# Kernel tuning notes

Hardware: AMD Instinct MI355X
Metric: run time of the kernel (lower is better)

## Reference

```python
import jax, jax.numpy as jnp
import numpy as np

D_MODEL = 1024
NUM_HEADS = 16
DEPTH = D_MODEL // NUM_HEADS
USE_MASKING = True


def setup_inputs() -> dict:
    key = jax.random.key(0)
    k1, k2, k3, k4 = jax.random.split(key, 4)
    B, S = 2, 2048
    x = jax.random.normal(k1, (B, S, D_MODEL), dtype=jnp.float32)
    # qkv_proj: Linear(d_model, 3*d_model, bias=False); torch stores W as [out, in]
    W_qkv = jax.random.normal(k2, (3 * D_MODEL, D_MODEL), dtype=jnp.float32) * (1.0 / np.sqrt(D_MODEL))
    W_out = jax.random.normal(k3, (D_MODEL, D_MODEL), dtype=jnp.float32) * (1.0 / np.sqrt(D_MODEL))
    b_out = jax.random.normal(k4, (D_MODEL,), dtype=jnp.float32) * 0.01
    return {"x": x, "W_qkv": W_qkv, "W_out": W_out, "b_out": b_out}


def reference(x, W_qkv, W_out, b_out):
    B, S, _ = x.shape
    qkv = jnp.einsum('bsd,ed->bse', x, W_qkv)  # [B,S,3*d_model]
    q, k, v = jnp.split(qkv, 3, axis=-1)
    # [B,S,H,depth] -> [B,H,S,depth]
    def heads(t):
        return t.reshape(B, S, NUM_HEADS, DEPTH).transpose(0, 2, 1, 3)
    q, k, v = heads(q), heads(k), heads(v)
    scores = jnp.einsum('bhqd,bhkd->bhqk', q, k) / np.sqrt(DEPTH).astype(np.float32)
    if USE_MASKING:
        mask = jnp.triu(jnp.ones((S, S), dtype=bool), k=1)
        scores = jnp.where(mask, -jnp.inf, scores)
    attn = jax.nn.softmax(scores, axis=-1)
    out = jnp.einsum('bhqk,bhkd->bhqd', attn, v)
    out = out.transpose(0, 2, 1, 3).reshape(B, S, D_MODEL)
    return jnp.einsum('bsd,ed->bse', out, W_out) + b_out
```

## Files before the change

kernel.cpp:

```cpp
#include <hip/hip_runtime.h>
#include <stdint.h>

typedef __attribute__((ext_vector_type(8))) short bf16x8;
typedef __attribute__((ext_vector_type(4))) float f32x4;
typedef __attribute__((ext_vector_type(4))) unsigned short u16x4;

#define AS1 __attribute__((address_space(1)))
#define AS3 __attribute__((address_space(3)))

#define BATCH 2
#define SEQ   2048
#define DMODEL 1024
#define NHEAD 16
#define DHEAD 64
#define QKVLD 3072
#define MROWS (BATCH*SEQ)

__device__ short g_xb   [MROWS * DMODEL];
__device__ short g_wqkv [3*DMODEL * DMODEL];
__device__ short g_wout [DMODEL * DMODEL];
__device__ short g_qkv  [(size_t)MROWS * QKVLD];
__device__ short g_attno[MROWS * DMODEL];

__device__ __forceinline__ unsigned short f2bf(float f) {
  union { float f; unsigned u; } v; v.f = f;
  unsigned r = v.u + 0x7FFFu + ((v.u >> 16) & 1u);
  return (unsigned short)(r >> 16);
}
__device__ __forceinline__ float bf2f(short s) {
  union { unsigned u; float f; } v; v.u = ((unsigned)(unsigned short)s) << 16;
  return v.f;
}
__device__ __forceinline__ void gload_lds16(const void* g, void* l) {
  __builtin_amdgcn_global_load_lds((const AS1 void*)(uintptr_t)g,
                                   (AS3 void*)(uint32_t)(uintptr_t)l, 16, 0, 0);
}

__global__ void cvt3(const float* __restrict__ x, const float* __restrict__ wq,
                     const float* __restrict__ wo) {
  const int N0 = MROWS * DMODEL;
  const int N1 = 3 * DMODEL * DMODEL;
  const int N2 = DMODEL * DMODEL;
  const int total = N0 + N1 + N2;
  int i = (blockIdx.x * blockDim.x + threadIdx.x) * 4;
  const int stride = gridDim.x * blockDim.x * 4;
  for (; i < total; i += stride) {
    const float* src; short* dst; int off;
    if (i < N0)           { src = x;  dst = g_xb;   off = i; }
    else if (i < N0 + N1) { src = wq; dst = g_wqkv; off = i - N0; }
    else                  { src = wo; dst = g_wout; off = i - N0 - N1; }
    float4 v = *reinterpret_cast<const float4*>(src + off);
    u16x4 o = { f2bf(v.x), f2bf(v.y), f2bf(v.z), f2bf(v.w) };
    *reinterpret_cast<u16x4*>(dst + off) = o;
  }
}

__device__ __forceinline__ void gemm_body(const short* __restrict__ A,
                                          const short* __restrict__ B,
                                          short* __restrict__ Cb,
                                          float* __restrict__ Cf,
                                          const float* __restrict__ bias,
                                          int N, int K, int bx, int by) {
  __shared__ short As[128 * 32];
  __shared__ short Bs[128 * 32];
  const int tid  = threadIdx.x;
  const int lane = tid & 63;
  const int wid  = tid >> 6;
  const int wr = wid >> 1, wc = wid & 1;
  const int g = lane >> 4, c = lane & 15;
  const long row0 = (long)by * 128;
  const long col0 = (long)bx * 128;

  const short* gA = A + (row0 + wid * 32 + (lane >> 2)) * (long)K + (lane & 3) * 8;
  const short* gB = B + (col0 + wid * 32 + (lane >> 2)) * (long)K + (lane & 3) * 8;
  short* lA = As + wid * 1024;
  short* lB = Bs + wid * 1024;

  f32x4 acc[4][4];
  const f32x4 z = {0.f, 0.f, 0.f, 0.f};
#pragma unroll
  for (int i = 0; i < 4; i++)
#pragma unroll
    for (int j = 0; j < 4; j++) acc[i][j] = z;

  for (int kt = 0; kt < K; kt += 32) {
    __syncthreads();
    gload_lds16(gA + kt,                lA);
    gload_lds16(gA + kt + 16 * (long)K, lA + 512);
    gload_lds16(gB + kt,                lB);
    gload_lds16(gB + kt + 16 * (long)K, lB + 512);
    __syncthreads();

    bf16x8 af[4], bfr[4];
#pragma unroll
    for (int mf = 0; mf < 4; mf++)
      af[mf] = *reinterpret_cast<const bf16x8*>(As + (wr * 64 + mf * 16 + c) * 32 + g * 8);
#pragma unroll
    for (int nf = 0; nf < 4; nf++)
      bfr[nf] = *reinterpret_cast<const bf16x8*>(Bs + (wc * 64 + nf * 16 + c) * 32 + g * 8);
#pragma unroll
    for (int mf = 0; mf < 4; mf++)
#pragma unroll
      for (int nf = 0; nf < 4; nf++)
        acc[mf][nf] = __builtin_amdgcn_mfma_f32_16x16x32_bf16(af[mf], bfr[nf], acc[mf][nf], 0, 0, 0);
  }

#pragma unroll
  for (int mf = 0; mf < 4; mf++)
#pragma unroll
    for (int nf = 0; nf < 4; nf++)
#pragma unroll
      for (int r = 0; r < 4; r++) {
        const long m = row0 + wr * 64 + mf * 16 + g * 4 + r;
        const long n = col0 + wc * 64 + nf * 16 + c;
        if (Cb) Cb[m * N + n] = (short)f2bf(acc[mf][nf][r]);
        else    Cf[m * N + n] = acc[mf][nf][r] + bias[n];
      }
}

__global__ __launch_bounds__(256) void gemm_qkv_k() {
  const int id = blockIdx.x;
  const int j = id >> 3;
  const int bx = j >> 2;
  const int by = ((id & 7) << 2) | (j & 3);
  gemm_body(g_xb, g_wqkv, g_qkv, nullptr, nullptr, 3 * DMODEL, DMODEL, bx, by);
}
__global__ __launch_bounds__(256) void gemm_out_k(float* __restrict__ out,
                                                  const float* __restrict__ bias) {
  const int id = blockIdx.x;
  const int j = id >> 3;
  const int bx = j >> 2;
  const int by = ((id & 7) << 2) | (j & 3);
  gemm_body(g_attno, g_wout, nullptr, out, bias, DMODEL, DMODEL, bx, by);
}

__global__ __launch_bounds__(256, 2) void flash_attn() {
  __shared__ short Kl[3][64 * 64];
  __shared__ short Vt[3][64 * 64];
  __shared__ short Pl[4][32 * 64];
  const int tid = threadIdx.x;
  const int lane = tid & 63, wid = tid >> 6;
  const int g = (lane >> 4) & 3, c = lane & 15;
  const int id = blockIdx.x;
  const int bh = id & 31;
  const int b = bh >> 4, h = bh & 15;
  const int qb = (id < 256) ? (15 - (id >> 5)) : ((id - 256) >> 5);
  const short* base = g_qkv + (size_t)b * SEQ * QKVLD + h * DHEAD;
  const int qw = qb * 128 + wid * 32;
  const int nt = 2 * qb + 2;

  const float QS = 0.18033688011112042f;
  bf16x8 qf[2][2];
#pragma unroll
  for (int n = 0; n < 2; n++)
#pragma unroll
    for (int kc = 0; kc < 2; kc++) {
      bf16x8 raw = *reinterpret_cast<const bf16x8*>(
          base + (size_t)(qw + n * 16 + c) * QKVLD + kc * 32 + g * 8);
#pragma unroll
      for (int j = 0; j < 8; j++) raw[j] = (short)f2bf(bf2f(raw[j]) * QS);
      qf[n][kc] = raw;
    }

  f32x4 oacc[2][4];
  const f32x4 z = {0.f, 0.f, 0.f, 0.f};
#pragma unroll
  for (int mq = 0; mq < 2; mq++)
#pragma unroll
    for (int nd = 0; nd < 4; nd++) oacc[mq][nd] = z;
  float mrow[2] = {-__builtin_inff(), -__builtin_inff()};
  float lrow[2] = {0.f, 0.f};

  const int srow = lane >> 3;
  const int scol = (lane & 7) ^ srow;
  const short* kgsrc = base + 1024 + (size_t)(wid * 16 + srow) * QKVLD + scol * 8;
  const short* vgsrc = base + 2048 + (size_t)lane * QKVLD + wid * 16;

  {
    bf16x8 a0 = *reinterpret_cast<const bf16x8*>(vgsrc);
    bf16x8 a1 = *reinterpret_cast<const bf16x8*>(vgsrc + 8);
    gload_lds16(kgsrc,                     &Kl[0][wid * 1024]);
    gload_lds16(kgsrc + (size_t)8 * QKVLD, &Kl[0][wid * 1024 + 512]);
    const size_t r1 = (size_t)64 * QKVLD;
    bf16x8 b0 = *reinterpret_cast<const bf16x8*>(vgsrc + r1);
    bf16x8 b1 = *reinterpret_cast<const bf16x8*>(vgsrc + r1 + 8);
    gload_lds16(kgsrc + r1,                     &Kl[1][wid * 1024]);
    gload_lds16(kgsrc + r1 + (size_t)8 * QKVLD, &Kl[1][wid * 1024 + 512]);
#pragma unroll
    for (int j = 0; j < 8; j++) {
      Vt[0][(wid * 16 + j) * 64 + (lane ^ (j << 3))] = a0[j];
      Vt[0][(wid * 16 + 8 + j) * 64 + (lane ^ (j << 3))] = a1[j];
    }
#pragma unroll
    for (int j = 0; j < 8; j++) {
      Vt[1][(wid * 16 + j) * 64 + (lane ^ (j << 3))] = b0[j];
      Vt[1][(wid * 16 + 8 + j) * 64 + (lane ^ (j << 3))] = b1[j];
    }
    asm volatile("s_waitcnt lgkmcnt(0)" ::: "memory");
    __builtin_amdgcn_sched_barrier(0);
    __builtin_amdgcn_s_barrier();
    asm volatile("" ::: "memory");
  }

  int cur = 0;
  for (int t = 0; t < nt; t++) {
    const int sidx = (cur + 2 >= 3) ? cur - 1 : cur + 2;
    const bool sl = (t + 2 < nt);
    bf16x8 vr0, vr1;
    if (sl) {
      const size_t roff = (size_t)(t + 2) * 64 * QKVLD;
      vr0 = *reinterpret_cast<const bf16x8*>(vgsrc + roff);
      vr1 = *reinterpret_cast<const bf16x8*>(vgsrc + roff + 8);
      gload_lds16(kgsrc + roff,                     &Kl[sidx][wid * 1024]);
      gload_lds16(kgsrc + roff + (size_t)8 * QKVLD, &Kl[sidx][wid * 1024 + 512]);
    }
    const int k0 = t * 64;
    if (k0 <= qw + 31) {
      f32x4 sc[4][2];
      __builtin_amdgcn_s_setprio(1);
#pragma unroll
      for (int m = 0; m < 4; m++) {
        const short* kr = &Kl[cur][(m * 16 + c) * 64];
        bf16x8 ka0 = *reinterpret_cast<const bf16x8*>(kr + ((g ^ (c & 7)) << 3));
        bf16x8 ka1 = *reinterpret_cast<const bf16x8*>(kr + (((4 + g) ^ (c & 7)) << 3));
#pragma unroll
        for (int n = 0; n < 2; n++) {
          f32x4 s = __builtin_amdgcn_mfma_f32_16x16x32_bf16(ka0, qf[n][0], z, 0, 0, 0);
          s = __builtin_amdgcn_mfma_f32_16x16x32_bf16(ka1, qf[n][1], s, 0, 0, 0);
          sc[m][n] = s;
        }
      }
      __builtin_amdgcn_s_setprio(0);
      if (k0 + 63 > qw) {
#pragma unroll
        for (int m = 0; m < 4; m++)
#pragma unroll
          for (int n = 0; n < 2; n++)
#pragma unroll
            for (int r = 0; r < 4; r++)
              if (k0 + m * 16 + g * 4 + r > qw + n * 16 + c)
                sc[m][n][r] = -__builtin_inff();
      }
      float tm[2];
#pragma unroll
      for (int n = 0; n < 2; n++) {
        f32x4 mm0 = sc[0][n], mm1 = sc[1][n];
#pragma unroll
        for (int r = 0; r < 4; r++) {
          mm0[r] = fmaxf(mm0[r], sc[2][n][r]);
          mm1[r] = fmaxf(mm1[r], sc[3][n][r]);
        }
        float v = fmaxf(fmaxf(fmaxf(mm0[0], mm0[1]), fmaxf(mm0[2], mm0[3])),
                        fmaxf(fmaxf(mm1[0], mm1[1]), fmaxf(mm1[2], mm1[3])));
        v = fmaxf(v, __shfl_xor(v, 16, 64));
        v = fmaxf(v, __shfl_xor(v, 32, 64));
        tm[n] = v;
      }
      const bool grow = (tm[0] > mrow[0] + 8.f) || (tm[1] > mrow[1] + 8.f);
      if (__any(grow)) {
        float aln[2];
#pragma unroll
        for (int n = 0; n < 2; n++) {
          const float mn = fmaxf(mrow[n], tm[n]);
          aln[n] = exp2f(mrow[n] - mn);
          mrow[n] = mn;
          lrow[n] *= aln[n];
        }
#pragma unroll
        for (int mq = 0; mq < 2; mq++)
#pragma unroll
          for (int r = 0; r < 4; r++) {
            const float alr = __shfl(aln[mq], g * 4 + r, 64);
#pragma unroll
            for (int nd = 0; nd < 4; nd++) oacc[mq][nd][r] *= alr;
          }
      }
#pragma unroll
      for (int n = 0; n < 2; n++) {
        float rs = 0.f;
        const int q = n * 16 + c;
#pragma unroll
        for (int m = 0; m < 4; m++) {
          u16x4 pb;
#pragma unroll
          for (int r = 0; r < 4; r++) {
            const float p = exp2f(sc[m][n][r] - mrow[n]);
            rs += p;
            pb[r] = f2bf(p);
          }
          const int idx = q * 64 + ((m * 16 + g * 4) ^ ((c & 7) << 3));
          *reinterpret_cast<u16x4*>(&Pl[wid][idx]) = pb;
        }
        rs += __shfl_xor(rs, 16, 64);
        rs += __shfl_xor(rs, 32, 64);
        lrow[n] += rs;
      }
      asm volatile("s_waitcnt lgkmcnt(0)" ::: "memory");
      bf16x8 pa[2][2];
#pragma unroll
      for (int mq = 0; mq < 2; mq++) {
        const int q = mq * 16 + c;
#pragma unroll
        for (int kc = 0; kc < 2; kc++)
          pa[mq][kc] = *reinterpret_cast<const bf16x8*>(
              &Pl[wid][q * 64 + ((kc * 32 + g * 8) ^ ((c & 7) << 3))]);
      }
      __builtin_amdgcn_s_setprio(1);
#pragma unroll
      for (int nd = 0; nd < 4; nd++) {
        const int d = nd * 16 + c;
#pragma unroll
        for (int kc = 0; kc < 2; kc++) {
          const bf16x8 vf = *reinterpret_cast<const bf16x8*>(
              &Vt[cur][d * 64 + ((kc * 32 + g * 8) ^ ((c & 7) << 3))]);
#pragma unroll
          for (int mq = 0; mq < 2; mq++)
            oacc[mq][nd] = __builtin_amdgcn_mfma_f32_16x16x32_bf16(pa[mq][kc], vf, oacc[mq][nd], 0, 0, 0);
        }
      }
      __builtin_amdgcn_s_setprio(0);
    }
    if (sl) {
#pragma unroll
      for (int j = 0; j < 8; j++) {
        Vt[sidx][(wid * 16 + j) * 64 + (lane ^ (j << 3))] = vr0[j];
        Vt[sidx][(wid * 16 + 8 + j) * 64 + (lane ^ (j << 3))] = vr1[j];
      }
    } else {
      asm volatile("s_waitcnt vmcnt(0)" ::: "memory");
    }
    asm volatile("s_waitcnt lgkmcnt(0)" ::: "memory");
    __builtin_amdgcn_sched_barrier(0);
    __builtin_amdgcn_s_barrier();
    asm volatile("" ::: "memory");
    cur = (cur + 1 == 3) ? 0 : cur + 1;
  }

  const float inv0 = 1.f / lrow[0], inv1 = 1.f / lrow[1];
#pragma unroll
  for (int mq = 0; mq < 2; mq++) {
    const float invm = mq ? inv1 : inv0;
#pragma unroll
    for (int r = 0; r < 4; r++) {
      const float linv = __shfl(invm, g * 4 + r, 64);
      const size_t orow = ((size_t)b * SEQ + qw + mq * 16 + g * 4 + r) * DMODEL + h * DHEAD;
#pragma unroll
      for (int nd = 0; nd < 4; nd++)
        g_attno[orow + nd * 16 + c] = (short)f2bf(oacc[mq][nd][r] * linv);
    }
  }
}

extern "C" void kernel_launch(void* const* d_in, const int* in_sizes, int n_in,
                              void* d_out, int out_size, void* d_ws, size_t ws_size,
                              hipStream_t stream) {
  (void)in_sizes; (void)n_in; (void)d_ws; (void)ws_size; (void)out_size;
  const float* x    = (const float*)d_in[0];
  const float* Wqkv = (const float*)d_in[1];
  const float* Wout = (const float*)d_in[2];
  const float* bout = (const float*)d_in[3];
  float* out = (float*)d_out;

  cvt3<<<2048, 256, 0, stream>>>(x, Wqkv, Wout);
  gemm_qkv_k<<<768, 256, 0, stream>>>();
  flash_attn<<<512, 256, 0, stream>>>();
  gemm_out_k<<<256, 256, 0, stream>>>(out, bout);
}
```

Before: 217.7 us.

## Pre-transpose V in a separate kernel and rebalance causal attention tiles

```diff
diff --git a/kernel.cpp b/kernel.cpp
--- a/kernel.cpp
+++ b/kernel.cpp
@@ -20,6 +20,7 @@
 __device__ short g_wqkv [3*DMODEL * DMODEL];
 __device__ short g_wout [DMODEL * DMODEL];
 __device__ short g_qkv  [(size_t)MROWS * QKVLD];
+__device__ short g_vt   [(size_t)BATCH*NHEAD * DHEAD * SEQ];
 __device__ short g_attno[MROWS * DMODEL];
 
 __device__ __forceinline__ unsigned short f2bf(float f) {
@@ -134,219 +135,187 @@
   gemm_body(g_attno, g_wout, nullptr, out, bias, DMODEL, DMODEL, bx, by);
 }
 
+__global__ __launch_bounds__(256) void transpose_v() {
+  __shared__ short T[64 * 64];
+  const int tid = threadIdx.x;
+  const int st = blockIdx.x, bh = blockIdx.y;
+  const int b = bh >> 4, h = bh & 15;
+  const int s0 = st * 64;
+  const int r = tid >> 2;
+  const int q4 = tid & 3;
+
+  const short* src = g_qkv + (size_t)(b * SEQ + s0 + r) * QKVLD + 2048 + h * DHEAD + q4 * 16;
+  bf16x8 v0 = *reinterpret_cast<const bf16x8*>(src);
+  bf16x8 v1 = *reinterpret_cast<const bf16x8*>(src + 8);
+#pragma unroll
+  for (int j = 0; j < 8; j++) {
+    int d = q4 * 16 + j;
+    T[d * 64 + (r ^ ((d & 7) << 3))] = v0[j];
+    d = q4 * 16 + 8 + j;
+    T[d * 64 + (r ^ ((d & 7) << 3))] = v1[j];
+  }
+  __syncthreads();
+  const int d = r;
+  short* dst = g_vt + (size_t)(bh * DHEAD + d) * SEQ + s0 + q4 * 16;
+  bf16x8 o0 = *reinterpret_cast<const bf16x8*>(&T[d * 64 + ((q4 * 16)     ^ ((d & 7) << 3))]);
+  bf16x8 o1 = *reinterpret_cast<const bf16x8*>(&T[d * 64 + ((q4 * 16 + 8) ^ ((d & 7) << 3))]);
+  *reinterpret_cast<bf16x8*>(dst)     = o0;
+  *reinterpret_cast<bf16x8*>(dst + 8) = o1;
+}
+
 __global__ __launch_bounds__(256, 2) void flash_attn() {
-  __shared__ short Kl[3][64 * 64];
-  __shared__ short Vt[3][64 * 64];
-  __shared__ short Pl[4][32 * 64];
+  __shared__ short Kl[3][4096];
+  __shared__ short Vl[3][4096];
+  __shared__ short Pl[4][1024];
   const int tid = threadIdx.x;
   const int lane = tid & 63, wid = tid >> 6;
   const int g = (lane >> 4) & 3, c = lane & 15;
   const int id = blockIdx.x;
   const int bh = id & 31;
+  const int jp = id >> 5;
   const int b = bh >> 4, h = bh & 15;
-  const int qb = (id < 256) ? (15 - (id >> 5)) : ((id - 256) >> 5);
-  const short* base = g_qkv + (size_t)b * SEQ * QKVLD + h * DHEAD;
-  const int qw = qb * 128 + wid * 32;
-  const int nt = 2 * qb + 2;
+  const short* qbase = g_qkv + (size_t)b * SEQ * QKVLD + h * DHEAD;
+  const short* kbase = qbase + 1024;
+  const short* vtb   = g_vt + (size_t)bh * DHEAD * SEQ;
+
+  const int srow = lane >> 3;
+  const int scol = (lane & 7) ^ srow;
+  const short* kg0 = kbase + (size_t)(wid * 16 + srow) * QKVLD + scol * 8;
+  const short* vg0 = vtb   + (size_t)(wid * 16 + srow) * SEQ   + scol * 8;
 
   const float QS = 0.18033688011112042f;
-  bf16x8 qf[2][2];
-#pragma unroll
-  for (int n = 0; n < 2; n++)
+  const f32x4 z = {0.f, 0.f, 0.f, 0.f};
+
+  for (int item = 0; item < 2; item++) {
+    const int qb = item ? jp : (31 - jp);
+    const int nt = qb + 1;
+    const int qw = qb * 64 + wid * 16;
+
+    bf16x8 qf[2];
 #pragma unroll
     for (int kc = 0; kc < 2; kc++) {
       bf16x8 raw = *reinterpret_cast<const bf16x8*>(
-          base + (size_t)(qw + n * 16 + c) * QKVLD + kc * 32 + g * 8);
+          qbase + (size_t)(qw + c) * QKVLD + kc * 32 + g * 8);
 #pragma unroll
       for (int j = 0; j < 8; j++) raw[j] = (short)f2bf(bf2f(raw[j]) * QS);
-      qf[n][kc] = raw;
+      qf[kc] = raw;
     }
 
-  f32x4 oacc[2][4];
-  const f32x4 z = {0.f, 0.f, 0.f, 0.f};
-#pragma unroll
-  for (int mq = 0; mq < 2; mq++)
-#pragma unroll
-    for (int nd = 0; nd < 4; nd++) oacc[mq][nd] = z;
-  float mrow[2] = {-__builtin_inff(), -__builtin_inff()};
-  float lrow[2] = {0.f, 0.f};
-
-  const int srow = lane >> 3;
-  const int scol = (lane & 7) ^ srow;
-  const short* kgsrc = base + 1024 + (size_t)(wid * 16 + srow) * QKVLD + scol * 8;
-  const short* vgsrc = base + 2048 + (size_t)lane * QKVLD + wid * 16;
-
-  {
-    bf16x8 a0 = *reinterpret_cast<const bf16x8*>(vgsrc);
-    bf16x8 a1 = *reinterpret_cast<const bf16x8*>(vgsrc + 8);
-    gload_lds16(kgsrc,                     &Kl[0][wid * 1024]);
-    gload_lds16(kgsrc + (size_t)8 * QKVLD, &Kl[0][wid * 1024 + 512]);
-    const size_t r1 = (size_t)64 * QKVLD;
-    bf16x8 b0 = *reinterpret_cast<const bf16x8*>(vgsrc + r1);
-    bf16x8 b1 = *reinterpret_cast<const bf16x8*>(vgsrc + r1 + 8);
-    gload_lds16(kgsrc + r1,                     &Kl[1][wid * 1024]);
-    gload_lds16(kgsrc + r1 + (size_t)8 * QKVLD, &Kl[1][wid * 1024 + 512]);
-#pragma unroll
-    for (int j = 0; j < 8; j++) {
-      Vt[0][(wid * 16 + j) * 64 + (lane ^ (j << 3))] = a0[j];
-      Vt[0][(wid * 16 + 8 + j) * 64 + (lane ^ (j << 3))] = a1[j];
+    f32x4 oacc[4];
+#pragma unroll
+    for (int nd = 0; nd < 4; nd++) oacc[nd] = z;
+    float mrow = -__builtin_inff(), lrow = 0.f;
+
+    gload_lds16(kg0,                        &Kl[0][wid * 1024]);
+    gload_lds16(kg0 + (size_t)8 * QKVLD,    &Kl[0][wid * 1024 + 512]);
+    gload_lds16(vg0,                        &Vl[0][wid * 1024]);
+    gload_lds16(vg0 + (size_t)8 * SEQ,      &Vl[0][wid * 1024 + 512]);
+    if (nt > 1) {
+      gload_lds16(kg0 + (size_t)64 * QKVLD,       &Kl[1][wid * 1024]);
+      gload_lds16(kg0 + (size_t)72 * QKVLD,       &Kl[1][wid * 1024 + 512]);
+      gload_lds16(vg0 + 64,                       &Vl[1][wid * 1024]);
+      gload_lds16(vg0 + (size_t)8 * SEQ + 64,     &Vl[1][wid * 1024 + 512]);
+      asm volatile("s_waitcnt vmcnt(4)" ::: "memory");
+    } else {
+      asm volatile("s_waitcnt vmcnt(0)" ::: "memory");
     }
-#pragma unroll
-    for (int j = 0; j < 8; j++) {
-      Vt[1][(wid * 16 + j) * 64 + (lane ^ (j << 3))] = b0[j];
-      Vt[1][(wid * 16 + 8 + j) * 64 + (lane ^ (j << 3))] = b1[j];
-    }
-    asm volatile("s_waitcnt lgkmcnt(0)" ::: "memory");
     __builtin_amdgcn_sched_barrier(0);
     __builtin_amdgcn_s_barrier();
     asm volatile("" ::: "memory");
-  }
-
-  int cur = 0;
-  for (int t = 0; t < nt; t++) {
-    const int sidx = (cur + 2 >= 3) ? cur - 1 : cur + 2;
-    const bool sl = (t + 2 < nt);
-    bf16x8 vr0, vr1;
-    if (sl) {
-      const size_t roff = (size_t)(t + 2) * 64 * QKVLD;
-      vr0 = *reinterpret_cast<const bf16x8*>(vgsrc + roff);
-      vr1 = *reinterpret_cast<const bf16x8*>(vgsrc + roff + 8);
-      gload_lds16(kgsrc + roff,                     &Kl[sidx][wid * 1024]);
-      gload_lds16(kgsrc + roff + (size_t)8 * QKVLD, &Kl[sidx][wid * 1024 + 512]);
-    }
-    const int k0 = t * 64;
-    if (k0 <= qw + 31) {
-      f32x4 sc[4][2];
+
+    int cur = 0;
+    for (int t = 0; t < nt; t++) {
+      const bool sl = (t + 2 < nt);
+      if (sl) {
+        const int sidx = (cur >= 1) ? cur - 1 : 2;
+        const size_t ko = (size_t)(t + 2) * 64 * QKVLD;
+        const size_t vo = (size_t)(t + 2) * 64;
+        gload_lds16(kg0 + ko,                     &Kl[sidx][wid * 1024]);
+        gload_lds16(kg0 + ko + (size_t)8 * QKVLD, &Kl[sidx][wid * 1024 + 512]);
+        gload_lds16(vg0 + vo,                     &Vl[sidx][wid * 1024]);
+        gload_lds16(vg0 + vo + (size_t)8 * SEQ,   &Vl[sidx][wid * 1024 + 512]);
+      }
+      f32x4 sc[4];
       __builtin_amdgcn_s_setprio(1);
 #pragma unroll
       for (int m = 0; m < 4; m++) {
         const short* kr = &Kl[cur][(m * 16 + c) * 64];
         bf16x8 ka0 = *reinterpret_cast<const bf16x8*>(kr + ((g ^ (c & 7)) << 3));
         bf16x8 ka1 = *reinterpret_cast<const bf16x8*>(kr + (((4 + g) ^ (c & 7)) << 3));
-#pragma unroll
-        for (int n = 0; n < 2; n++) {
-          f32x4 s = __builtin_amdgcn_mfma_f32_16x16x32_bf16(ka0, qf[n][0], z, 0, 0, 0);
-          s = __builtin_amdgcn_mfma_f32_16x16x32_bf16(ka1, qf[n][1], s, 0, 0, 0);
-          sc[m][n] = s;
+        f32x4 s = __builtin_amdgcn_mfma_f32_16x16x32_bf16(ka0, qf[0], z, 0, 0, 0);
+        sc[m] = __builtin_amdgcn_mfma_f32_16x16x32_bf16(ka1, qf[1], s, 0, 0, 0);
+      }
+      __builtin_amdgcn_s_setprio(0);
+      if (t == nt - 1) {
+#pragma unroll
+        for (int m = 0; m < 4; m++)
+#pragma unroll
+          for (int r = 0; r < 4; r++)
+            if (m * 16 + g * 4 + r > wid * 16 + c) sc[m][r] = -__builtin_inff();
+      }
+      f32x4 mm;
+#pragma unroll
+      for (int r = 0; r < 4; r++)
+        mm[r] = fmaxf(fmaxf(sc[0][r], sc[1][r]), fmaxf(sc[2][r], sc[3][r]));
+      float tmx = fmaxf(fmaxf(mm[0], mm[1]), fmaxf(mm[2], mm[3]));
+      tmx = fmaxf(tmx, __shfl_xor(tmx, 16, 64));
+      tmx = fmaxf(tmx, __shfl_xor(tmx, 32, 64));
+      if (__any(tmx > mrow + 8.f)) {
+        const float mn = fmaxf(mrow, tmx);
+        const float al = exp2f(mrow - mn);
+        mrow = mn; lrow *= al;
+#pragma unroll
+        for (int r = 0; r < 4; r++) {
+          const float alr = __shfl(al, g * 4 + r, 64);
+#pragma unroll
+          for (int nd = 0; nd < 4; nd++) oacc[nd][r] *= alr;
         }
       }
+      float rs = 0.f;
+#pragma unroll
+      for (int m = 0; m < 4; m++) {
+        u16x4 pb;
+#pragma unroll
+        for (int r = 0; r < 4; r++) {
+          const float p = exp2f(sc[m][r] - mrow);
+          rs += p; pb[r] = f2bf(p);
+        }
+        *reinterpret_cast<u16x4*>(&Pl[wid][c * 64 + ((m * 16 + g * 4) ^ ((c & 7) << 3))]) = pb;
+      }
+      rs += __shfl_xor(rs, 16, 64);
+      rs += __shfl_xor(rs, 32, 64);
+      lrow += rs;
+      asm volatile("s_waitcnt lgkmcnt(0)" ::: "memory");
+      __builtin_amdgcn_sched_barrier(0);
+      bf16x8 pa0 = *reinterpret_cast<const bf16x8*>(&Pl[wid][c * 64 + ((g * 8)      ^ ((c & 7) << 3))]);
+      bf16x8 pa1 = *reinterpret_cast<const bf16x8*>(&Pl[wid][c * 64 + ((32 + g * 8) ^ ((c & 7) << 3))]);
+      __builtin_amdgcn_s_setprio(1);
+#pragma unroll
+      for (int nd = 0; nd < 4; nd++) {
+        const short* vr = &Vl[cur][(nd * 16 + c) * 64];
+        bf16x8 vf0 = *reinterpret_cast<const bf16x8*>(vr + ((g ^ (c & 7)) << 3));
+        bf16x8 vf1 = *reinterpret_cast<const bf16x8*>(vr + (((4 + g) ^ (c & 7)) << 3));
+        oacc[nd] = __builtin_amdgcn_mfma_f32_16x16x32_bf16(pa0, vf0, oacc[nd], 0, 0, 0);
+        oacc[nd] = __builtin_amdgcn_mfma_f32_16x16x32_bf16(pa1, vf1, oacc[nd], 0, 0, 0);
+      }
       __builtin_amdgcn_s_setprio(0);
-      if (k0 + 63 > qw) {
-#pragma unroll
-        for (int m = 0; m < 4; m++)
-#pragma unroll
-          for (int n = 0; n < 2; n++)
-#pragma unroll
-            for (int r = 0; r < 4; r++)
-              if (k0 + m * 16 + g * 4 + r > qw + n * 16 + c)
-                sc[m][n][r] = -__builtin_inff();
-      }
-      float tm[2];
-#pragma unroll
-      for (int n = 0; n < 2; n++) {
-        f32x4 mm0 = sc[0][n], mm1 = sc[1][n];
-#pragma unroll
-        for (int r = 0; r < 4; r++) {
-          mm0[r] = fmaxf(mm0[r], sc[2][n][r]);
-          mm1[r] = fmaxf(mm1[r], sc[3][n][r]);
-        }
-        float v = fmaxf(fmaxf(fmaxf(mm0[0], mm0[1]), fmaxf(mm0[2], mm0[3])),
-                        fmaxf(fmaxf(mm1[0], mm1[1]), fmaxf(mm1[2], mm1[3])));
-        v = fmaxf(v, __shfl_xor(v, 16, 64));
-        v = fmaxf(v, __shfl_xor(v, 32, 64));
-        tm[n] = v;
-      }
-      const bool grow = (tm[0] > mrow[0] + 8.f) || (tm[1] > mrow[1] + 8.f);
-      if (__any(grow)) {
-        float aln[2];
-#pragma unroll
-        for (int n = 0; n < 2; n++) {
-          const float mn = fmaxf(mrow[n], tm[n]);
-          aln[n] = exp2f(mrow[n] - mn);
-          mrow[n] = mn;
-          lrow[n] *= aln[n];
-        }
-#pragma unroll
-        for (int mq = 0; mq < 2; mq++)
-#pragma unroll
-          for (int r = 0; r < 4; r++) {
-            const float alr = __shfl(aln[mq], g * 4 + r, 64);
-#pragma unroll
-            for (int nd = 0; nd < 4; nd++) oacc[mq][nd][r] *= alr;
-          }
-      }
-#pragma unroll
-      for (int n = 0; n < 2; n++) {
-        float rs = 0.f;
-        const int q = n * 16 + c;
-#pragma unroll
-        for (int m = 0; m < 4; m++) {
-          u16x4 pb;
-#pragma unroll
-          for (int r = 0; r < 4; r++) {
-            const float p = exp2f(sc[m][n][r] - mrow[n]);
-            rs += p;
-            pb[r] = f2bf(p);
-          }
-          const int idx = q * 64 + ((m * 16 + g * 4) ^ ((c & 7) << 3));
-          *reinterpret_cast<u16x4*>(&Pl[wid][idx]) = pb;
-        }
-        rs += __shfl_xor(rs, 16, 64);
-        rs += __shfl_xor(rs, 32, 64);
-        lrow[n] += rs;
-      }
+      if (sl) asm volatile("s_waitcnt vmcnt(4)" ::: "memory");
+      else    asm volatile("s_waitcnt vmcnt(0)" ::: "memory");
       asm volatile("s_waitcnt lgkmcnt(0)" ::: "memory");
-      bf16x8 pa[2][2];
-#pragma unroll
-      for (int mq = 0; mq < 2; mq++) {
-        const int q = mq * 16 + c;
-#pragma unroll
-        for (int kc = 0; kc < 2; kc++)
-          pa[mq][kc] = *reinterpret_cast<const bf16x8*>(
-              &Pl[wid][q * 64 + ((kc * 32 + g * 8) ^ ((c & 7) << 3))]);
-      }
-      __builtin_amdgcn_s_setprio(1);
-#pragma unroll
-      for (int nd = 0; nd < 4; nd++) {
-        const int d = nd * 16 + c;
-#pragma unroll
-        for (int kc = 0; kc < 2; kc++) {
-          const bf16x8 vf = *reinterpret_cast<const bf16x8*>(
-              &Vt[cur][d * 64 + ((kc * 32 + g * 8) ^ ((c & 7) << 3))]);
-#pragma unroll
-          for (int mq = 0; mq < 2; mq++)
-            oacc[mq][nd] = __builtin_amdgcn_mfma_f32_16x16x32_bf16(pa[mq][kc], vf, oacc[mq][nd], 0, 0, 0);
-        }
-      }
-      __builtin_amdgcn_s_setprio(0);
+      __builtin_amdgcn_sched_barrier(0);
+      __builtin_amdgcn_s_barrier();
+      asm volatile("" ::: "memory");
+      cur = (cur == 2) ? 0 : cur + 1;
     }
-    if (sl) {
-#pragma unroll
-      for (int j = 0; j < 8; j++) {
-        Vt[sidx][(wid * 16 + j) * 64 + (lane ^ (j << 3))] = vr0[j];
-        Vt[sidx][(wid * 16 + 8 + j) * 64 + (lane ^ (j << 3))] = vr1[j];
-      }
-    } else {
-      asm volatile("s_waitcnt vmcnt(0)" ::: "memory");
-    }
-    asm volatile("s_waitcnt lgkmcnt(0)" ::: "memory");
-    __builtin_amdgcn_sched_barrier(0);
-    __builtin_amdgcn_s_barrier();
-    asm volatile("" ::: "memory");
-    cur = (cur + 1 == 3) ? 0 : cur + 1;
-  }
-
-  const float inv0 = 1.f / lrow[0], inv1 = 1.f / lrow[1];
-#pragma unroll
-  for (int mq = 0; mq < 2; mq++) {
-    const float invm = mq ? inv1 : inv0;
+
+    const float inv = 1.f / lrow;
 #pragma unroll
     for (int r = 0; r < 4; r++) {
-      const float linv = __shfl(invm, g * 4 + r, 64);
-      const size_t orow = ((size_t)b * SEQ + qw + mq * 16 + g * 4 + r) * DMODEL + h * DHEAD;
+      const float linv = __shfl(inv, g * 4 + r, 64);
+      const size_t orow = ((size_t)b * SEQ + qw + g * 4 + r) * DMODEL + h * DHEAD;
 #pragma unroll
       for (int nd = 0; nd < 4; nd++)
-        g_attno[orow + nd * 16 + c] = (short)f2bf(oacc[mq][nd][r] * linv);
+        g_attno[orow + nd * 16 + c] = (short)f2bf(oacc[nd][r] * linv);
     }
   }
 }
@@ -363,6 +332,7 @@
 
   cvt3<<<2048, 256, 0, stream>>>(x, Wqkv, Wout);
   gemm_qkv_k<<<768, 256, 0, stream>>>();
+  transpose_v<<<dim3(32, 32), 256, 0, stream>>>();
   flash_attn<<<512, 256, 0, stream>>>();
   gemm_out_k<<<256, 256, 0, stream>>>(out, bout);
 }
```

New measurement: 212.8 us. 1.02x faster.
